# Kernel optimization log

Hardware: AMD Instinct MI355X
Metric: run time of the kernel (lower is better)

Reference implementation:

```python
import jax, jax.numpy as jnp
import numpy as np
from jax import lax

N = 131072

# ---- soft logic gates on {0,1}-valued floats ----
def XOR(a, b): return a + b - 2.0 * a * b
def AND(a, b): return a * b
def OR(a, b):  return a + b - a * b
def NOT(a):    return 1.0 - a
def MUX(sel, a, b):  # sel==1 -> a, sel==0 -> b
    return sel * a + (1.0 - sel) * b
def and_tree(x): return jnp.prod(x, axis=-1, keepdims=True)
def or_tree(x):  return 1.0 - jnp.prod(1.0 - x, axis=-1, keepdims=True)

def ripple_sub(a, b):
    """a - b on LSB-first bit vectors [..., n]; returns (diff_bits, borrow_out [...,1])."""
    at = jnp.moveaxis(a, -1, 0)
    bt = jnp.moveaxis(b, -1, 0)
    def step(borrow, ab):
        ai, bi = ab
        axb = XOR(ai, bi)
        d = XOR(axb, borrow)
        bout = OR(AND(NOT(ai), bi), AND(NOT(axb), borrow))
        return bout, d
    b0 = jnp.zeros(a.shape[:-1], a.dtype)
    bout, d = lax.scan(step, b0, (at, bt))
    return jnp.moveaxis(d, 0, -1), bout[..., None]

def ripple_add(a, b):
    """a + b on LSB-first bit vectors [..., n]; returns (sum_bits, carry_out [...,1])."""
    at = jnp.moveaxis(a, -1, 0)
    bt = jnp.moveaxis(b, -1, 0)
    def step(c, ab):
        ai, bi = ab
        axb = XOR(ai, bi)
        s = XOR(axb, c)
        cout = OR(AND(ai, bi), AND(axb, c))
        return cout, s
    c0 = jnp.zeros(a.shape[:-1], a.dtype)
    cout, s = lax.scan(step, c0, (at, bt))
    return jnp.moveaxis(s, 0, -1), cout[..., None]

def div_iteration(R_lsb, D_lsb):
    """Restoring division step. R,D LSB-first [...,55]. Returns (q_bit [...,1], R_next_lsb)."""
    R_trial, borrow = ripple_sub(R_lsb, D_lsb)
    q = NOT(borrow)
    R_next = MUX(borrow, R_lsb, R_trial)
    return q, R_next

def _forward(A, B):
    A, B = jnp.broadcast_arrays(A, B)
    bs = A.shape[:-1]
    dt = A.dtype
    z1 = jnp.zeros(bs + (1,), dt)
    o1 = jnp.ones(bs + (1,), dt)

    s_a, e_a, m_a = A[..., 0:1], A[..., 1:12], A[..., 12:64]
    s_b, e_b, m_b = B[..., 0:1], B[..., 1:12], B[..., 12:64]

    s_out = XOR(s_a, s_b)

    # ---- special-case detection ----
    e_a_all_one, e_b_all_one = and_tree(e_a), and_tree(e_b)
    e_a_is_zero, e_b_is_zero = NOT(or_tree(e_a)), NOT(or_tree(e_b))
    m_a_any, m_b_any = or_tree(m_a), or_tree(m_b)
    m_a_is_zero, m_b_is_zero = NOT(m_a_any), NOT(m_b_any)
    a_is_zero = AND(e_a_is_zero, m_a_is_zero)
    b_is_zero = AND(e_b_is_zero, m_b_is_zero)
    a_is_inf = AND(e_a_all_one, m_a_is_zero)
    b_is_inf = AND(e_b_all_one, m_b_is_zero)
    a_is_nan = AND(e_a_all_one, m_a_any)
    b_is_nan = AND(e_b_all_one, m_b_any)
    either_nan = OR(a_is_nan, b_is_nan)
    div_by_zero = AND(NOT(a_is_zero), b_is_zero)
    zero_div_zero = AND(a_is_zero, b_is_zero)
    inf_div_inf = AND(a_is_inf, b_is_inf)
    result_is_nan = OR(either_nan, OR(zero_div_zero, inf_div_inf))
    inf_div_y = AND(a_is_inf, NOT(b_is_inf))
    result_is_inf = OR(div_by_zero, inf_div_y)
    zero_div_x = AND(a_is_zero, NOT(b_is_zero))
    x_div_inf = AND(NOT(a_is_inf), b_is_inf)
    result_is_zero = OR(zero_div_x, x_div_inf)

    # ---- exponent: e_a - e_b + 1023 (13-bit LSB-first) ----
    e_a_13 = jnp.concatenate([e_a[..., ::-1], z1, z1], axis=-1)
    e_b_13 = jnp.concatenate([e_b[..., ::-1], z1, z1], axis=-1)
    exp_diff, _ = ripple_sub(e_a_13, e_b_13)
    const_1023 = jnp.concatenate([o1] * 10 + [z1] * 3, axis=-1)
    exp_result, _ = ripple_add(exp_diff, const_1023)

    # ---- 57-step restoring division of 55-bit mantissas (MSB-first registers) ----
    A_55 = jnp.concatenate([z1, o1, m_a, z1], axis=-1)  # [0 | 1.m_a | 0]
    D_55 = jnp.concatenate([z1, o1, m_b, z1], axis=-1)
    D_lsb = D_55[..., ::-1]

    def div_step(R, _):
        q, R_sub_lsb = div_iteration(R[..., ::-1], D_lsb)
        R_sub = R_sub_lsb[..., ::-1]
        R_next = jnp.concatenate([R_sub[..., 1:], z1], axis=-1)  # shift left
        return R_next, q[..., 0]

    R_carry, qs = lax.scan(div_step, A_55, jnp.arange(56))
    q_last, R_last_lsb = div_iteration(R_carry[..., ::-1], D_lsb)
    R = R_last_lsb[..., ::-1]
    Q_raw = jnp.concatenate([jnp.moveaxis(qs, 0, -1), q_last], axis=-1)  # [...,57]

    # ---- normalize + RNE rounding ----
    q0 = Q_raw[..., 0:1]
    need_normalize = NOT(q0)
    remainder_nonzero = or_tree(R)
    mant_normal = Q_raw[..., 1:53]
    round_normal = Q_raw[..., 53:54]
    sticky_normal = or_tree(jnp.concatenate([Q_raw[..., 54:57], remainder_nonzero], axis=-1))
    mant_shifted = Q_raw[..., 2:54]
    round_shifted = Q_raw[..., 54:55]
    sticky_shifted = or_tree(jnp.concatenate([Q_raw[..., 55:57], remainder_nonzero], axis=-1))
    mant_52 = MUX(q0, mant_normal, mant_shifted)
    round_bit = MUX(q0, round_normal, round_shifted)
    sticky_bit = MUX(q0, sticky_normal, sticky_shifted)

    const_1_13 = jnp.concatenate([o1] + [z1] * 12, axis=-1)
    exp_minus1, _ = ripple_sub(exp_result, const_1_13)
    exp_adjusted = MUX(need_normalize, exp_minus1, exp_result)

    lsb = mant_52[..., -1:]
    round_up = AND(round_bit, OR(sticky_bit, lsb))
    mant_53_lsb = jnp.concatenate([mant_52[..., ::-1], z1], axis=-1)
    round_inc_lsb = jnp.concatenate([round_up] + [z1] * 52, axis=-1)
    mant_rounded_lsb, carry = ripple_add(mant_53_lsb, round_inc_lsb)
    mant_final = mant_rounded_lsb[..., :52][..., ::-1]

    exp_plus1, _ = ripple_add(exp_adjusted, const_1_13)
    exp_final_13 = MUX(carry, exp_plus1, exp_adjusted)
    zero_52 = jnp.zeros(bs + (52,), dt)
    mant_final = MUX(carry, zero_52, mant_final)

    exp_final = exp_final_13[..., :11][..., ::-1]
    is_overflow = or_tree(exp_final_13[..., 11:13])
    exp_is_zero = NOT(or_tree(exp_final_13))
    exp_sign = exp_final_13[..., 12:13]
    is_underflow = OR(exp_sign, exp_is_zero)

    result = jnp.concatenate([s_out, exp_final, mant_final], axis=-1)

    # ---- special-value muxes ----
    ones11 = jnp.ones(bs + (11,), dt)
    nan_mant = jnp.concatenate([o1] + [z1] * 51, axis=-1)
    nan_val = jnp.concatenate([s_out, ones11, nan_mant], axis=-1)
    inf_val = jnp.concatenate([s_out, ones11, zero_52], axis=-1)
    zero_val = jnp.concatenate([s_out, jnp.zeros(bs + (11,), dt), zero_52], axis=-1)

    result = MUX(result_is_nan, nan_val, result)
    not_nan = NOT(result_is_nan)
    is_inf_valid = AND(result_is_inf, not_nan)
    result = MUX(is_inf_valid, inf_val, result)
    not_inf = NOT(result_is_inf)
    is_zero_valid = AND(result_is_zero, AND(not_nan, not_inf))
    result = MUX(is_zero_valid, zero_val, result)
    overflow_valid = AND(is_overflow, AND(not_nan, AND(not_inf, NOT(result_is_zero))))
    result = MUX(overflow_valid, inf_val, result)
    underflow_valid = AND(is_underflow, AND(not_nan, AND(not_inf, AND(NOT(is_overflow), NOT(result_is_zero)))))
    result = MUX(underflow_valid, zero_val, result)
    return result


def setup_inputs() -> dict:
    key = jax.random.key(0)
    kA, kB = jax.random.split(key)
    A = jax.random.randint(kA, (N, 64), 0, 2).astype(jnp.float32)
    B = jax.random.randint(kB, (N, 64), 0, 2).astype(jnp.float32)
    return {"A": A, "B": B}


def reference(A, B):
    return _forward(A, B)
```

## Files before the change

### kernel.cpp

```cpp
#include <hip/hip_runtime.h>
#include <stdint.h>

#define M52 0xFFFFFFFFFFFFFULL

__device__ __forceinline__ uint64_t shfl64(uint64_t x, int src) {
    int lo = __shfl((int)(uint32_t)x, src, 64);
    int hi = __shfl((int)(uint32_t)(x >> 32), src, 64);
    return ((uint64_t)(uint32_t)hi << 32) | (uint64_t)(uint32_t)lo;
}

__global__ __launch_bounds__(256) void fp64div_kernel(
    const float* __restrict__ A, const float* __restrict__ B,
    float* __restrict__ out, int n_rows)
{
    const int tid  = blockIdx.x * blockDim.x + threadIdx.x;
    const int lane = threadIdx.x & 63;
    const int wave_base = tid & ~63;
    if (wave_base >= n_rows) return;

    const float* Ap = A + (size_t)wave_base * 64 + lane;
    const float* Bp = B + (size_t)wave_base * 64 + lane;

    uint64_t my_a = 0, my_b = 0;
    #pragma unroll
    for (int rb = 0; rb < 64; rb += 16) {
        float va[16], vb[16];
        #pragma unroll
        for (int i = 0; i < 16; ++i) va[i] = Ap[(size_t)(rb + i) * 64];
        #pragma unroll
        for (int i = 0; i < 16; ++i) vb[i] = Bp[(size_t)(rb + i) * 64];
        #pragma unroll
        for (int i = 0; i < 16; ++i) {
            uint64_t ma = __ballot(va[i] != 0.0f);
            if (lane == rb + i) my_a = ma;
            uint64_t mb = __ballot(vb[i] != 0.0f);
            if (lane == rb + i) my_b = mb;
        }
    }

    const uint64_t av = __brevll(my_a);
    const uint64_t bv = __brevll(my_b);

    const uint32_t sa = (uint32_t)(av >> 63), sb = (uint32_t)(bv >> 63);
    const uint32_t s_out = sa ^ sb;
    const uint32_t Ea = (uint32_t)(av >> 52) & 0x7FFu;
    const uint32_t Eb = (uint32_t)(bv >> 52) & 0x7FFu;
    const uint64_t Ma = av & M52;
    const uint64_t Mb = bv & M52;

    const bool ea_all1 = (Ea == 0x7FFu), eb_all1 = (Eb == 0x7FFu);
    const bool ea_zero = (Ea == 0u),     eb_zero = (Eb == 0u);
    const bool ma_zero = (Ma == 0ull),   mb_zero = (Mb == 0ull);
    const bool a_zero = ea_zero && ma_zero, b_zero = eb_zero && mb_zero;
    const bool a_inf  = ea_all1 && ma_zero, b_inf  = eb_all1 && mb_zero;
    const bool a_nan  = ea_all1 && !ma_zero, b_nan = eb_all1 && !mb_zero;

    const bool r_nan  = a_nan || b_nan || (a_zero && b_zero) || (a_inf && b_inf);
    const bool r_inf  = (!a_zero && b_zero) || (a_inf && !b_inf);
    const bool r_zero = (a_zero && !b_zero) || (!a_inf && b_inf);

    const uint32_t exp13 = (Ea - Eb + 1023u) & 0x1FFFu;

    uint64_t R = (1ULL << 53) | (Ma << 1);
    const uint64_t D = (1ULL << 53) | (Mb << 1);
    uint64_t Q = 0;
    #pragma unroll
    for (int i = 0; i < 56; ++i) {
        const bool ge = (R >= D);
        const uint64_t t = R - D;
        R = ge ? t : R;
        Q = (Q << 1) | (ge ? 1u : 0u);
        R <<= 1;
    }
    {
        const bool ge = (R >= D);
        const uint64_t t = R - D;
        R = ge ? t : R;
        Q = (Q << 1) | (ge ? 1u : 0u);
    }

    const uint32_t q0 = (uint32_t)(Q >> 56) & 1u;
    const uint32_t rem_nz = (R != 0ull) ? 1u : 0u;

    const uint64_t mant52 = q0 ? ((Q >> 4) & M52) : ((Q >> 3) & M52);
    const uint32_t rbit   = q0 ? ((uint32_t)(Q >> 3) & 1u) : ((uint32_t)(Q >> 2) & 1u);
    const uint32_t sticky = (q0 ? (((Q & 7ull) != 0ull) ? 1u : 0u)
                                : (((Q & 3ull) != 0ull) ? 1u : 0u)) | rem_nz;
    const uint32_t exp_f  = q0 ? exp13 : ((exp13 - 1u) & 0x1FFFu);

    const uint32_t lsb = (uint32_t)mant52 & 1u;
    const uint32_t rup = rbit & (sticky | lsb);
    const uint64_t mant_final = (mant52 + rup) & M52;

    const uint32_t exp11    = exp_f & 0x7FFu;
    const bool overflow  = (exp_f >> 11) != 0u;
    const bool underflow = (((exp_f >> 12) & 1u) != 0u) || (exp_f == 0u);

    uint64_t res = ((uint64_t)s_out << 63) | ((uint64_t)exp11 << 52) | mant_final;
    const uint64_t zero_v = ((uint64_t)s_out << 63);
    const uint64_t inf_v  = zero_v | (0x7FFULL << 52);
    const uint64_t nan_v  = inf_v | (1ULL << 51);

    if (r_nan)        res = nan_v;
    else if (r_inf)   res = inf_v;
    else if (r_zero)  res = zero_v;
    else if (overflow) res = inf_v;
    else if (underflow) res = zero_v;

    const uint64_t out_word = __brevll(res);

    float* Op = out + (size_t)wave_base * 64 + lane;
    #pragma unroll 8
    for (int r = 0; r < 64; ++r) {
        const uint64_t w = shfl64(out_word, r);
        Op[(size_t)r * 64] = (float)((uint32_t)(w >> lane) & 1u);
    }
}

extern "C" void kernel_launch(void* const* d_in, const int* in_sizes, int n_in,
                              void* d_out, int out_size, void* d_ws, size_t ws_size,
                              hipStream_t stream) {
    const float* A = (const float*)d_in[0];
    const float* B = (const float*)d_in[1];
    float* out = (float*)d_out;
    const int n_rows = in_sizes[0] / 64;
    const int threads = 256;
    const int blocks = (n_rows + threads - 1) / threads;
    fp64div_kernel<<<blocks, threads, 0, stream>>>(A, B, out, n_rows);
}
```

Measured before the change: 101.8 us.

## Load each row per thread with vector loads instead of wave ballot transpose

Each thread now reads its own 256-byte row of A and B with sixteen 128-bit loads each. It packs the bits by testing bit 29 of each float, instead of using a wave-wide strided load plus 128 ballots to transpose the bits. The output is likewise written as sixteen 128-bit stores of 1.0f/0.0f masks per thread, replacing 64 two-part shuffles. This removes the cross-lane ballot and shuffle overhead. In exchange, each load and store instruction touches lanes 256 bytes apart instead of coalescing, and the kernel holds many more VGPRs live. The bit-29 test assumes inputs are exactly 0.0 or 1.0.

```diff
diff --git a/kernel.cpp b/kernel.cpp
--- a/kernel.cpp
+++ b/kernel.cpp
@@ -3,43 +3,48 @@
 
 #define M52 0xFFFFFFFFFFFFFULL
 
-__device__ __forceinline__ uint64_t shfl64(uint64_t x, int src) {
-    int lo = __shfl((int)(uint32_t)x, src, 64);
-    int hi = __shfl((int)(uint32_t)(x >> 32), src, 64);
-    return ((uint64_t)(uint32_t)hi << 32) | (uint64_t)(uint32_t)lo;
-}
+__global__ __launch_bounds__(256) void fp64div_kernel(
+    const uint4* __restrict__ A, const uint4* __restrict__ B,
+    uint4* __restrict__ out, int n_rows)
+{
+    const int row = blockIdx.x * blockDim.x + threadIdx.x;
+    if (row >= n_rows) return;
 
-__global__ __launch_bounds__(256) void fp64div_kernel(
-    const float* __restrict__ A, const float* __restrict__ B,
-    float* __restrict__ out, int n_rows)
-{
-    const int tid  = blockIdx.x * blockDim.x + threadIdx.x;
-    const int lane = threadIdx.x & 63;
-    const int wave_base = tid & ~63;
-    if (wave_base >= n_rows) return;
+    const uint4* ap = A + (size_t)row * 16;
+    const uint4* bp = B + (size_t)row * 16;
 
-    const float* Ap = A + (size_t)wave_base * 64 + lane;
-    const float* Bp = B + (size_t)wave_base * 64 + lane;
+    uint4 va[16], vb[16];
+    #pragma unroll
+    for (int j = 0; j < 16; ++j) va[j] = ap[j];
+    #pragma unroll
+    for (int j = 0; j < 16; ++j) vb[j] = bp[j];
 
-    uint64_t my_a = 0, my_b = 0;
+    uint32_t alo = 0u, ahi = 0u, blo = 0u, bhi = 0u;
     #pragma unroll
-    for (int rb = 0; rb < 64; rb += 16) {
-        float va[16], vb[16];
-        #pragma unroll
-        for (int i = 0; i < 16; ++i) va[i] = Ap[(size_t)(rb + i) * 64];
-        #pragma unroll
-        for (int i = 0; i < 16; ++i) vb[i] = Bp[(size_t)(rb + i) * 64];
-        #pragma unroll
-        for (int i = 0; i < 16; ++i) {
-            uint64_t ma = __ballot(va[i] != 0.0f);
-            if (lane == rb + i) my_a = ma;
-            uint64_t mb = __ballot(vb[i] != 0.0f);
-            if (lane == rb + i) my_b = mb;
-        }
+    for (int j = 0; j < 8; ++j) {
+        alo |= ((va[j].x >> 29) & 1u) << (4 * j + 0);
+        alo |= ((va[j].y >> 29) & 1u) << (4 * j + 1);
+        alo |= ((va[j].z >> 29) & 1u) << (4 * j + 2);
+        alo |= ((va[j].w >> 29) & 1u) << (4 * j + 3);
+        blo |= ((vb[j].x >> 29) & 1u) << (4 * j + 0);
+        blo |= ((vb[j].y >> 29) & 1u) << (4 * j + 1);
+        blo |= ((vb[j].z >> 29) & 1u) << (4 * j + 2);
+        blo |= ((vb[j].w >> 29) & 1u) << (4 * j + 3);
+    }
+    #pragma unroll
+    for (int j = 8; j < 16; ++j) {
+        ahi |= ((va[j].x >> 29) & 1u) << (4 * j - 32);
+        ahi |= ((va[j].y >> 29) & 1u) << (4 * j - 31);
+        ahi |= ((va[j].z >> 29) & 1u) << (4 * j - 30);
+        ahi |= ((va[j].w >> 29) & 1u) << (4 * j - 29);
+        bhi |= ((vb[j].x >> 29) & 1u) << (4 * j - 32);
+        bhi |= ((vb[j].y >> 29) & 1u) << (4 * j - 31);
+        bhi |= ((vb[j].z >> 29) & 1u) << (4 * j - 30);
+        bhi |= ((vb[j].w >> 29) & 1u) << (4 * j - 29);
     }
 
-    const uint64_t av = __brevll(my_a);
-    const uint64_t bv = __brevll(my_b);
+    const uint64_t av = __brevll(((uint64_t)ahi << 32) | alo);
+    const uint64_t bv = __brevll(((uint64_t)bhi << 32) | blo);
 
     const uint32_t sa = (uint32_t)(av >> 63), sb = (uint32_t)(bv >> 63);
     const uint32_t s_out = sa ^ sb;
@@ -92,7 +97,7 @@
     const uint32_t rup = rbit & (sticky | lsb);
     const uint64_t mant_final = (mant52 + rup) & M52;
 
-    const uint32_t exp11    = exp_f & 0x7FFu;
+    const uint32_t exp11   = exp_f & 0x7FFu;
     const bool overflow  = (exp_f >> 11) != 0u;
     const bool underflow = (((exp_f >> 12) & 1u) != 0u) || (exp_f == 0u);
 
@@ -101,28 +106,36 @@
     const uint64_t inf_v  = zero_v | (0x7FFULL << 52);
     const uint64_t nan_v  = inf_v | (1ULL << 51);
 
-    if (r_nan)        res = nan_v;
-    else if (r_inf)   res = inf_v;
-    else if (r_zero)  res = zero_v;
-    else if (overflow) res = inf_v;
+    if (r_nan)          res = nan_v;
+    else if (r_inf)     res = inf_v;
+    else if (r_zero)    res = zero_v;
+    else if (overflow)  res = inf_v;
     else if (underflow) res = zero_v;
 
-    const uint64_t out_word = __brevll(res);
+    const uint64_t ow = __brevll(res);
+    const uint32_t owlo = (uint32_t)ow;
+    const uint32_t owhi = (uint32_t)(ow >> 32);
 
-    float* Op = out + (size_t)wave_base * 64 + lane;
-    #pragma unroll 8
-    for (int r = 0; r < 64; ++r) {
-        const uint64_t w = shfl64(out_word, r);
-        Op[(size_t)r * 64] = (float)((uint32_t)(w >> lane) & 1u);
+    uint4* op = out + (size_t)row * 16;
+    #pragma unroll
+    for (int j = 0; j < 16; ++j) {
+        const uint32_t w = (j < 8) ? owlo : owhi;
+        const int base = (4 * j) & 31;
+        uint4 o;
+        o.x = 0x3F800000u & (uint32_t)((int32_t)(w << (31 - (base + 0))) >> 31);
+        o.y = 0x3F800000u & (uint32_t)((int32_t)(w << (31 - (base + 1))) >> 31);
+        o.z = 0x3F800000u & (uint32_t)((int32_t)(w << (31 - (base + 2))) >> 31);
+        o.w = 0x3F800000u & (uint32_t)((int32_t)(w << (31 - (base + 3))) >> 31);
+        op[j] = o;
     }
 }
 
 extern "C" void kernel_launch(void* const* d_in, const int* in_sizes, int n_in,
                               void* d_out, int out_size, void* d_ws, size_t ws_size,
                               hipStream_t stream) {
-    const float* A = (const float*)d_in[0];
-    const float* B = (const float*)d_in[1];
-    float* out = (float*)d_out;
+    const uint4* A = (const uint4*)d_in[0];
+    const uint4* B = (const uint4*)d_in[1];
+    uint4* out = (uint4*)d_out;
     const int n_rows = in_sizes[0] / 64;
     const int threads = 256;
     const int blocks = (n_rows + threads - 1) / threads;
```

Result: slower. 128.7 us (+26.5%).

## Use 128-bit loads/stores and LDS bit-packing instead of per-row ballots

Applied to the files above, without the earlier changes.

Switches the global loads and stores to uint4 (four floats per lane). Input bits are extracted from the float exponent bit, staged through shared memory as nibbles, and compacted into 64-bit words. This replaces the 128 ballots per wave and the 64 scalar shuffle stores with 16 vector stores. The intent is to cut memory-instruction count and cross-lane overhead in a bandwidth-bound kernel. It relies on inputs being exactly 0.0 or 1.0, because it tests bit 29 of each float, and it adds an LDS round trip plus an occupancy hint.

```diff
diff --git a/kernel.cpp b/kernel.cpp
--- a/kernel.cpp
+++ b/kernel.cpp
@@ -3,46 +3,17 @@
 
 #define M52 0xFFFFFFFFFFFFFULL
 
-__device__ __forceinline__ uint64_t shfl64(uint64_t x, int src) {
+__device__ __forceinline__ uint64_t shfl64v(uint64_t x, int src) {
     int lo = __shfl((int)(uint32_t)x, src, 64);
     int hi = __shfl((int)(uint32_t)(x >> 32), src, 64);
     return ((uint64_t)(uint32_t)hi << 32) | (uint64_t)(uint32_t)lo;
 }
 
-__global__ __launch_bounds__(256) void fp64div_kernel(
-    const float* __restrict__ A, const float* __restrict__ B,
-    float* __restrict__ out, int n_rows)
-{
-    const int tid  = blockIdx.x * blockDim.x + threadIdx.x;
-    const int lane = threadIdx.x & 63;
-    const int wave_base = tid & ~63;
-    if (wave_base >= n_rows) return;
+__device__ __forceinline__ uint64_t circuit_divide(uint64_t pa, uint64_t pb) {
+    const uint64_t av = __brevll(pa);
+    const uint64_t bv = __brevll(pb);
 
-    const float* Ap = A + (size_t)wave_base * 64 + lane;
-    const float* Bp = B + (size_t)wave_base * 64 + lane;
-
-    uint64_t my_a = 0, my_b = 0;
-    #pragma unroll
-    for (int rb = 0; rb < 64; rb += 16) {
-        float va[16], vb[16];
-        #pragma unroll
-        for (int i = 0; i < 16; ++i) va[i] = Ap[(size_t)(rb + i) * 64];
-        #pragma unroll
-        for (int i = 0; i < 16; ++i) vb[i] = Bp[(size_t)(rb + i) * 64];
-        #pragma unroll
-        for (int i = 0; i < 16; ++i) {
-            uint64_t ma = __ballot(va[i] != 0.0f);
-            if (lane == rb + i) my_a = ma;
-            uint64_t mb = __ballot(vb[i] != 0.0f);
-            if (lane == rb + i) my_b = mb;
-        }
-    }
-
-    const uint64_t av = __brevll(my_a);
-    const uint64_t bv = __brevll(my_b);
-
-    const uint32_t sa = (uint32_t)(av >> 63), sb = (uint32_t)(bv >> 63);
-    const uint32_t s_out = sa ^ sb;
+    const uint32_t s_out = (uint32_t)((av ^ bv) >> 63);
     const uint32_t Ea = (uint32_t)(av >> 52) & 0x7FFu;
     const uint32_t Eb = (uint32_t)(bv >> 52) & 0x7FFu;
     const uint64_t Ma = av & M52;
@@ -92,7 +63,7 @@
     const uint32_t rup = rbit & (sticky | lsb);
     const uint64_t mant_final = (mant52 + rup) & M52;
 
-    const uint32_t exp11    = exp_f & 0x7FFu;
+    const uint32_t exp11   = exp_f & 0x7FFu;
     const bool overflow  = (exp_f >> 11) != 0u;
     const bool underflow = (((exp_f >> 12) & 1u) != 0u) || (exp_f == 0u);
 
@@ -101,30 +72,86 @@
     const uint64_t inf_v  = zero_v | (0x7FFULL << 52);
     const uint64_t nan_v  = inf_v | (1ULL << 51);
 
-    if (r_nan)        res = nan_v;
-    else if (r_inf)   res = inf_v;
-    else if (r_zero)  res = zero_v;
-    else if (overflow) res = inf_v;
+    if (r_nan)          res = nan_v;
+    else if (r_inf)     res = inf_v;
+    else if (r_zero)    res = zero_v;
+    else if (overflow)  res = inf_v;
     else if (underflow) res = zero_v;
 
-    const uint64_t out_word = __brevll(res);
+    return __brevll(res);
+}
 
-    float* Op = out + (size_t)wave_base * 64 + lane;
-    #pragma unroll 8
-    for (int r = 0; r < 64; ++r) {
-        const uint64_t w = shfl64(out_word, r);
-        Op[(size_t)r * 64] = (float)((uint32_t)(w >> lane) & 1u);
+__device__ __forceinline__ uint32_t compact16(uint32_t d) {
+    uint32_t t = (d | (d >> 4)) & 0x00FF00FFu;
+    return (t | (t >> 8)) & 0x0000FFFFu;
+}
+
+__global__ __launch_bounds__(256, 2) void fp64div_kernel(
+    const uint4* __restrict__ A, const uint4* __restrict__ B,
+    uint4* __restrict__ out, int n_rows)
+{
+    __shared__ uint8_t lds[4][2][1024];
+    const int tid  = blockIdx.x * blockDim.x + threadIdx.x;
+    const int lane = threadIdx.x & 63;
+    const int wid  = threadIdx.x >> 6;
+    const int wave = tid >> 6;
+    if ((wave << 6) >= n_rows) return;
+
+    const size_t chunk = (size_t)wave * 1024;
+    const uint4* Ap = A + chunk + lane;
+    const uint4* Bp = B + chunk + lane;
+
+    uint4 va[16], vb[16];
+    #pragma unroll
+    for (int i = 0; i < 16; ++i) va[i] = Ap[i * 64];
+    #pragma unroll
+    for (int i = 0; i < 16; ++i) vb[i] = Bp[i * 64];
+
+    uint8_t* la = lds[wid][0];
+    uint8_t* lb = lds[wid][1];
+    #pragma unroll
+    for (int i = 0; i < 16; ++i) {
+        const uint32_t na = ((va[i].x >> 29) & 1u) | ((va[i].y >> 28) & 2u)
+                          | ((va[i].z >> 27) & 4u) | ((va[i].w >> 26) & 8u);
+        la[i * 64 + lane] = (uint8_t)na;
+        const uint32_t nb = ((vb[i].x >> 29) & 1u) | ((vb[i].y >> 28) & 2u)
+                          | ((vb[i].z >> 27) & 4u) | ((vb[i].w >> 26) & 8u);
+        lb[i * 64 + lane] = (uint8_t)nb;
+    }
+
+    const uint4 ra = ((const uint4*)la)[lane];
+    const uint4 rb = ((const uint4*)lb)[lane];
+    const uint64_t pa = (uint64_t)(compact16(ra.x) | (compact16(ra.y) << 16))
+                      | ((uint64_t)(compact16(ra.z) | (compact16(ra.w) << 16)) << 32);
+    const uint64_t pb = (uint64_t)(compact16(rb.x) | (compact16(rb.y) << 16))
+                      | ((uint64_t)(compact16(rb.z) | (compact16(rb.w) << 16)) << 32);
+
+    const uint64_t w = circuit_divide(pa, pb);
+
+    uint4* Op = out + chunk + lane;
+    const int s0   = 4 * (lane & 15);
+    const int srcb = lane >> 4;
+    #pragma unroll
+    for (int i = 0; i < 16; ++i) {
+        const uint64_t wr = shfl64v(w, srcb + 4 * i);
+        const uint32_t nib = (uint32_t)(wr >> s0) & 0xFu;
+        uint4 o;
+        o.x = (nib & 1u) ? 0x3F800000u : 0u;
+        o.y = (nib & 2u) ? 0x3F800000u : 0u;
+        o.z = (nib & 4u) ? 0x3F800000u : 0u;
+        o.w = (nib & 8u) ? 0x3F800000u : 0u;
+        Op[i * 64] = o;
     }
 }
 
 extern "C" void kernel_launch(void* const* d_in, const int* in_sizes, int n_in,
                               void* d_out, int out_size, void* d_ws, size_t ws_size,
                               hipStream_t stream) {
-    const float* A = (const float*)d_in[0];
-    const float* B = (const float*)d_in[1];
-    float* out = (float*)d_out;
+    const uint4* A = (const uint4*)d_in[0];
+    const uint4* B = (const uint4*)d_in[1];
+    uint4* out = (uint4*)d_out;
     const int n_rows = in_sizes[0] / 64;
     const int threads = 256;
-    const int blocks = (n_rows + threads - 1) / threads;
+    const int blocks = (n_rows + (threads - 1)) / threads;
     fp64div_kernel<<<blocks, threads, 0, stream>>>(A, B, out, n_rows);
 }
```

Measured after the change: 99.04 us. 1.03x faster.
